# Performance work log

Measured on AMD Instinct MI355X. Metric: run time of the kernel, lower is better.

Reference implementation:

```python
import jax, jax.numpy as jnp
import numpy as np

B, T, S, E, H, V = 64, 72, 72, 128, 256, 32000


def setup_inputs() -> dict:
    key = jax.random.key(0)
    ks = jax.random.split(key, 12)
    scale = 1.0 / np.sqrt(H)
    return {
        "target_tensor": jax.random.randint(ks[0], (B, T), 0, V),
        "encoder_outputs": jax.random.normal(ks[1], (B, S, H), dtype=jnp.float32),
        "encoder_seq_lens": jax.random.randint(ks[2], (B,), 1, S + 1),
        "h0": jax.random.normal(ks[3], (B, H), dtype=jnp.float32),
        "c0": jax.random.normal(ks[4], (B, H), dtype=jnp.float32),
        "emb": jax.random.normal(ks[5], (V, E), dtype=jnp.float32) * 0.05,
        "W_ih": jax.random.uniform(ks[6], (4 * H, E), jnp.float32, -scale, scale),
        "W_hh": jax.random.uniform(ks[7], (4 * H, H), jnp.float32, -scale, scale),
        "b_ih": jax.random.uniform(ks[8], (4 * H,), jnp.float32, -scale, scale),
        "b_hh": jax.random.uniform(ks[9], (4 * H,), jnp.float32, -scale, scale),
        "W_lin": jax.random.uniform(ks[10], (V, 2 * H), jnp.float32, -scale, scale),
        "b_lin": jax.random.uniform(ks[11], (V,), jnp.float32, -scale, scale),
    }


def reference(target_tensor, encoder_outputs, encoder_seq_lens, h0, c0,
              emb, W_ih, W_hh, b_ih, b_hh, W_lin, b_lin):
    # attention mask over encoder positions: (B, S) bool
    mask = jnp.arange(S)[None, :] < encoder_seq_lens[:, None]
    inv_sqrt_h = 1.0 / jnp.sqrt(jnp.asarray(H, jnp.float32))
    bias = b_ih + b_hh

    def step(carry, tok):
        h, c = carry                                   # (B,H) each
        x = emb[tok]                                   # (B,E) embedding lookup
        gates = x @ W_ih.T + h @ W_hh.T + bias         # (B,4H), torch gate order i,f,g,o
        i, f, g, o = jnp.split(gates, 4, axis=-1)
        c_new = jax.nn.sigmoid(f) * c + jax.nn.sigmoid(i) * jnp.tanh(g)
        h_new = jax.nn.sigmoid(o) * jnp.tanh(c_new)    # lstm_output for a 1-step LSTM
        scores = jnp.einsum('bh,bsh->bs', h_new, encoder_outputs) * inv_sqrt_h
        scores = jnp.where(mask, scores, -jnp.inf)
        attn = jax.nn.softmax(scores, axis=-1)         # (B,S)
        ctx = jnp.einsum('bs,bsh->bh', attn, encoder_outputs)
        logits = jnp.concatenate([h_new, ctx], axis=-1) @ W_lin.T + b_lin  # (B,V)
        return (h_new, c_new), logits

    (_, _), outs = jax.lax.scan(step, (h0, c0), target_tensor.T)  # outs: (T,B,V)
    return jnp.transpose(outs, (1, 0, 2))              # (B, T, V)
```

## Files before the change

### kernel.cpp

```cpp
#include <hip/hip_runtime.h>

#define BB 64
#define TT 72
#define SS 72
#define EE 128
#define HH 256
#define VV 32000
#define KK 512
#define NB 4
#define NATTN 64
#define NGEMM 188
#define NCHUNK 36
#define NNT 125
#define NITEM (NCHUNK * NNT)

using f32x4  = __attribute__((ext_vector_type(4))) float;
using short8 = __attribute__((ext_vector_type(8))) short;
typedef unsigned long long u64;

__device__ __forceinline__ unsigned short f2bf(float f) {
  unsigned u = __float_as_uint(f);
  unsigned r = (u + 0x7fffu + ((u >> 16) & 1u)) >> 16;
  return (unsigned short)r;
}
__device__ __forceinline__ float bf2f(unsigned short b) {
  return __uint_as_float(((unsigned)b) << 16);
}
__device__ __forceinline__ float sigm(float x) { return 1.f / (1.f + __expf(-x)); }
__device__ __forceinline__ float tanh_f(float x) { return 1.f - 2.f / (__expf(2.f * x) + 1.f); }

__device__ __forceinline__ float wsum(float v) {
  v += __shfl_xor(v, 1, 64);  v += __shfl_xor(v, 2, 64);  v += __shfl_xor(v, 4, 64);
  v += __shfl_xor(v, 8, 64);  v += __shfl_xor(v, 16, 64); v += __shfl_xor(v, 32, 64);
  return v;
}
__device__ __forceinline__ float wmax(float v) {
  v = fmaxf(v, __shfl_xor(v, 1, 64));  v = fmaxf(v, __shfl_xor(v, 2, 64));
  v = fmaxf(v, __shfl_xor(v, 4, 64));  v = fmaxf(v, __shfl_xor(v, 8, 64));
  v = fmaxf(v, __shfl_xor(v, 16, 64)); v = fmaxf(v, __shfl_xor(v, 32, 64));
  return v;
}
__device__ __forceinline__ void g2l16(const void* g, void* l) {
  __builtin_amdgcn_global_load_lds((const __attribute__((address_space(1))) void*)g,
                                   (__attribute__((address_space(3))) void*)l, 16, 0, 0);
}
__device__ __forceinline__ uint4 pack8(const float4 v0, const float4 v1) {
  uint4 o;
  o.x = f2bf(v0.x) | ((unsigned)f2bf(v0.y) << 16);
  o.y = f2bf(v0.z) | ((unsigned)f2bf(v0.w) << 16);
  o.z = f2bf(v1.x) | ((unsigned)f2bf(v1.y) << 16);
  o.w = f2bf(v1.z) | ((unsigned)f2bf(v1.w) << 16);
  return o;
}
__device__ __forceinline__ u64 aload(const u64* p) {
  return __hip_atomic_load(p, __ATOMIC_RELAXED, __HIP_MEMORY_SCOPE_AGENT);
}
__device__ __forceinline__ void astore(u64* p, u64 v) {
  __hip_atomic_store(p, v, __ATOMIC_RELAXED, __HIP_MEMORY_SCOPE_AGENT);
}

__global__ void prep_kernel(const int* __restrict__ tok, const float* __restrict__ emb,
                            const float* __restrict__ Wlin,
                            uint4* __restrict__ xembt, unsigned short* __restrict__ wlin16) {
  const int bid = blockIdx.x, tid = threadIdx.x;
  if (bid < 18) {
    for (int e = bid * 256 + tid; e < TT * 16 * 64; e += 18 * 256) {
      const int b = e & 63, kcx = (e >> 6) & 15, t = e >> 10;
      const int tk = tok[b * TT + t];
      const float4* s = (const float4*)(emb + (size_t)tk * EE + kcx * 8);
      xembt[e] = pack8(s[0], s[1]);
    }
  } else {
    const int n4 = (VV * KK) / 4;
    for (int i = (bid - 18) * 256 + tid; i < n4; i += 238 * 256) {
      float4 v = ((const float4*)Wlin)[i];
      ushort4 o;
      o.x = f2bf(v.x); o.y = f2bf(v.y); o.z = f2bf(v.z); o.w = f2bf(v.w);
      ((ushort4*)wlin16)[i] = o;
    }
  }
}

__global__ __launch_bounds__(512) void mega_kernel(
    const float* __restrict__ h0, const float* __restrict__ c0,
    const float* __restrict__ Wih, const float* __restrict__ Whh,
    const float* __restrict__ bih, const float* __restrict__ bhh,
    const float* __restrict__ enc, const int* __restrict__ lens,
    const float* __restrict__ blin, const uint4* __restrict__ xembt,
    const unsigned short* __restrict__ wlin16,
    uint4* __restrict__ hex, unsigned int* __restrict__ sync,
    u64* __restrict__ hcat64, float* __restrict__ out) {
  __shared__ __align__(16) char smem[114688];
  __shared__ int s_role;

  const int tid = threadIdx.x;
  unsigned int* flags1 = sync;
  unsigned int* F2     = sync + 8;
  unsigned int* elect  = sync + 96;

  if (tid == 0) {
    unsigned xcd;
    asm volatile("s_getreg_b32 %0, hwreg(20, 0, 8)" : "=s"(xcd));
    xcd &= 7;
    int role = -1;
    const unsigned my = __hip_atomic_fetch_add(elect + xcd, 1u,
                          __ATOMIC_RELAXED, __HIP_MEMORY_SCOPE_AGENT);
    if (my < NB) {
      if (my == NB - 1) {
        unsigned exp = 0;
        __hip_atomic_compare_exchange_strong(elect + 8, &exp, xcd + 1,
            __ATOMIC_RELAXED, __ATOMIC_RELAXED, __HIP_MEMORY_SCOPE_AGENT);
      }
      unsigned wv;
      while ((wv = __hip_atomic_load(elect + 8, __ATOMIC_RELAXED,
                                     __HIP_MEMORY_SCOPE_AGENT)) == 0)
        __builtin_amdgcn_s_sleep(1);
      if (wv == xcd + 1) role = (int)my;
    }
    if (role < 0) {
      const unsigned idx = __hip_atomic_fetch_add(elect + 9, 1u,
                             __ATOMIC_RELAXED, __HIP_MEMORY_SCOPE_AGENT);
      role = (idx < NATTN) ? (100 + (int)idx) : (1000 + (int)(idx - NATTN));
    }
    s_role = role;
  }
  __syncthreads();
  const int role = s_role;

  if (role < NB) {
    const int bk = role;
    uint4* hx = (uint4*)smem;
    uint4* xw = (uint4*)(smem + 49152);
    const int ln = tid & 63, w = tid >> 6;
    const int n16 = ln & 15, kgrp = ln >> 4;
    const int wj = w >> 1, wb = w & 1;
    u64* hexq = (u64*)hex;

    short8 wf[4][8];
    f32x4 biasf[4];
    {
      const int jrow = bk * 64 + wj * 16;
#pragma unroll
      for (int g = 0; g < 4; ++g) {
        const int row = g * HH + jrow + n16;
#pragma unroll
        for (int kt = 0; kt < 8; ++kt) {
          const float* src = Whh + (size_t)row * HH + kt * 32 + kgrp * 8;
          const float4 v0 = ((const float4*)src)[0];
          const float4 v1 = ((const float4*)src)[1];
          short8 wv;
          wv[0]=(short)f2bf(v0.x); wv[1]=(short)f2bf(v0.y); wv[2]=(short)f2bf(v0.z); wv[3]=(short)f2bf(v0.w);
          wv[4]=(short)f2bf(v1.x); wv[5]=(short)f2bf(v1.y); wv[6]=(short)f2bf(v1.z); wv[7]=(short)f2bf(v1.w);
          wf[g][kt] = wv;
        }
        const int r4 = g * HH + jrow + kgrp * 4;
        const float4 bi = *(const float4*)(bih + r4);
        const float4 bh = *(const float4*)(bhh + r4);
        biasf[g] = (f32x4){bi.x + bh.x, bi.y + bh.y, bi.z + bh.z, bi.w + bh.w};
      }
    }
#pragma unroll
    for (int i = 0; i < 8; ++i) {
      const int e = i * 512 + tid;
      const int en = e & 15, ek = (e >> 4) & 3, ewj = (e >> 6) & 3,
                ekt = (e >> 8) & 3, eg = e >> 10;
      const int row = eg * HH + bk * 64 + ewj * 16 + en;
      const float* src = Wih + (size_t)row * EE + ekt * 32 + ek * 8;
      xw[e] = pack8(((const float4*)src)[0], ((const float4*)src)[1]);
    }
    float creg[2][4];
#pragma unroll
    for (int mt = 0; mt < 2; ++mt)
#pragma unroll
      for (int r = 0; r < 4; ++r)
        creg[mt][r] = c0[(size_t)((wb * 2 + mt) * 16 + n16) * HH + bk * 64 + wj * 16 + kgrp * 4 + r];
#pragma unroll
    for (int i = 0; i < 4; ++i) {
      const int e = i * 512 + tid;
      const int kc = e >> 6, b = e & 63;
      const float* src = h0 + (size_t)b * HH + kc * 8;
      hx[kc * 64 + b] = pack8(((const float4*)src)[0], ((const float4*)src)[1]);
    }
    __syncthreads();

    const int kcq  = bk * 8 + wj * 2 + (kgrp >> 1);
    const int half = kgrp & 1;
    const int jq   = bk * 16 + wj * 4 + kgrp;

    for (int t = 0; t < TT; ++t) {
#pragma unroll
      for (int i = 0; i < 2; ++i) {
        const int e = (i * 8 + w) * 64 + ln;
        g2l16(xembt + (size_t)t * 1024 + e, (char*)&hx[32 * 64] + e * 16);
      }
      if (t > 0) {
        if (tid < NB) {
          while (__hip_atomic_load(flags1 + tid, __ATOMIC_RELAXED,
                                   __HIP_MEMORY_SCOPE_AGENT) < (unsigned)t)
            __builtin_amdgcn_s_sleep(1);
        }
        __syncthreads();
#pragma unroll
        for (int i = 0; i < 4; ++i) {
          const int e = (i * 8 + w) * 64 + ln;
          g2l16(hex + (size_t)t * 2048 + e, (char*)hx + e * 16);
        }
      }
      __syncthreads();

      f32x4 acc[4][2];
#pragma unroll
      for (int g = 0; g < 4; ++g)
#pragma unroll
        for (int mt = 0; mt < 2; ++mt)
          acc[g][mt] = biasf[g];

#pragma unroll
      for (int kt = 0; kt < 8; ++kt) {
#pragma unroll
        for (int mt = 0; mt < 2; ++mt) {
          const short8 b = *(const short8*)&hx[(kt * 4 + kgrp) * 64 + (wb * 2 + mt) * 16 + n16];
          acc[0][mt] = __builtin_amdgcn_mfma_f32_16x16x32_bf16(wf[0][kt], b, acc[0][mt], 0, 0, 0);
          acc[1][mt] = __builtin_amdgcn_mfma_f32_16x16x32_bf16(wf[1][kt], b, acc[1][mt], 0, 0, 0);
          acc[2][mt] = __builtin_amdgcn_mfma_f32_16x16x32_bf16(wf[2][kt], b, acc[2][mt], 0, 0, 0);
          acc[3][mt] = __builtin_amdgcn_mfma_f32_16x16x32_bf16(wf[3][kt], b, acc[3][mt], 0, 0, 0);
        }
      }
#pragma unroll
      for (int kti = 0; kti < 4; ++kti) {
        short8 wx[4];
#pragma unroll
        for (int g = 0; g < 4; ++g)
          wx[g] = *(const short8*)&xw[(((g * 4 + kti) * 4 + wj) * 4 + kgrp) * 16 + n16];
#pragma unroll
        for (int mt = 0; mt < 2; ++mt) {
          const short8 b = *(const short8*)&hx[(32 + kti * 4 + kgrp) * 64 + (wb * 2 + mt) * 16 + n16];
#pragma unroll
          for (int g = 0; g < 4; ++g)
            acc[g][mt] = __builtin_amdgcn_mfma_f32_16x16x32_bf16(wx[g], b, acc[g][mt], 0, 0, 0);
        }
      }

#pragma unroll
      for (int mt = 0; mt < 2; ++mt) {
        u64 pk = 0;
#pragma unroll
        for (int r = 0; r < 4; ++r) {
          const float iv = acc[0][mt][r], fv = acc[1][mt][r],
                      gv = acc[2][mt][r], ov = acc[3][mt][r];
          const float cn = sigm(fv) * creg[mt][r] + sigm(iv) * tanh_f(gv);
          creg[mt][r] = cn;
          const float hv = sigm(ov) * tanh_f(cn);
          pk |= (u64)f2bf(hv) << (16 * r);
        }
        const int batch = (wb * 2 + mt) * 16 + n16;
        astore(hexq + ((size_t)((t + 1) * 32 + kcq) * 64 + batch) * 2 + half, pk);
        astore(hcat64 + (size_t)(t * 64 + batch) * 128 + jq, pk);
      }
      asm volatile("s_waitcnt vmcnt(0)" ::: "memory");
      __syncthreads();
      if (tid == 0)
        __hip_atomic_store(flags1 + bk, (unsigned)(t + 1),
                           __ATOMIC_RELAXED, __HIP_MEMORY_SCOPE_AGENT);
    }
  } else if (role < 1000) {
    const int b = role - 100;
    float* enc_s = (float*)smem;
    float* h_s   = (float*)(smem + 73728);
    float* at_s  = (float*)(smem + 74752);
    float* ctx_s = (float*)(smem + 75776);
    const int wv8 = tid >> 6, ln = tid & 63;
    const int len = lens[b];
    const u64* hexq = (const u64*)hex;
    {
      const float4* src = (const float4*)(enc + (size_t)b * SS * HH);
      float4* dst = (float4*)enc_s;
      for (int i = tid; i < SS * HH / 4; i += 512) dst[i] = src[i];
    }
    __syncthreads();

    for (int t = 0; t < TT; ++t) {
      if (tid < NB) {
        while (__hip_atomic_load(flags1 + tid, __ATOMIC_RELAXED,
                                 __HIP_MEMORY_SCOPE_AGENT) < (unsigned)(t + 1))
          __builtin_amdgcn_s_sleep(1);
      }
      __syncthreads();
      if (tid < 64) {
        const int kc = tid >> 1, hf = tid & 1;
        const u64 v = aload(hexq + ((size_t)((t + 1) * 32 + kc) * 64 + b) * 2 + hf);
        const int j0 = kc * 8 + hf * 4;
        h_s[j0]     = bf2f((unsigned short)v);
        h_s[j0 + 1] = bf2f((unsigned short)(v >> 16));
        h_s[j0 + 2] = bf2f((unsigned short)(v >> 32));
        h_s[j0 + 3] = bf2f((unsigned short)(v >> 48));
      }
      __syncthreads();

      const float4 hv = ((const float4*)h_s)[ln];
      for (int s = wv8; s < SS; s += 8) {
        const float4 ev = ((const float4*)(enc_s + s * HH))[ln];
        float p = hv.x * ev.x + hv.y * ev.y + hv.z * ev.z + hv.w * ev.w;
        p = wsum(p);
        if (ln == 0) at_s[s] = p * 0.0625f;
      }
      __syncthreads();
      if (wv8 == 0) {
        const float v0 = (ln < len) ? at_s[ln] : -3.0e38f;
        const bool has1 = (ln < 8) && (64 + ln < len);
        const float v1 = has1 ? at_s[64 + ln] : -3.0e38f;
        const float m = wmax(fmaxf(v0, v1));
        const float e0 = (ln < len) ? __expf(v0 - m) : 0.f;
        const float e1 = has1 ? __expf(v1 - m) : 0.f;
        const float inv = 1.f / wsum(e0 + e1);
        at_s[ln] = e0 * inv;
        if (ln < 8) at_s[64 + ln] = e1 * inv;
      }
      __syncthreads();
      if (tid < HH) {
        float acc = 0.f;
#pragma unroll 8
        for (int s = 0; s < SS; ++s) acc += at_s[s] * enc_s[s * HH + tid];
        ctx_s[tid] = acc;
      }
      __syncthreads();
      if (tid < 64) {
        const u64 pk = (u64)f2bf(ctx_s[tid * 4])
                     | ((u64)f2bf(ctx_s[tid * 4 + 1]) << 16)
                     | ((u64)f2bf(ctx_s[tid * 4 + 2]) << 32)
                     | ((u64)f2bf(ctx_s[tid * 4 + 3]) << 48);
        astore(hcat64 + (size_t)(t * 64 + b) * 128 + 64 + tid, pk);
      }
      asm volatile("s_waitcnt vmcnt(0)" ::: "memory");
      __syncthreads();
      if (tid == 0)
        __hip_atomic_fetch_add(F2 + t, 1u, __ATOMIC_RELAXED, __HIP_MEMORY_SCOPE_AGENT);
    }
  } else {
    const int gid = role - 1000;
    unsigned short* As = (unsigned short*)smem;
    unsigned short* Bs = (unsigned short*)(smem + 8192);
    char* Asb = smem;
    char* Bsb = smem + 8192;
    const int ln = tid & 63, w = tid >> 6;
    const int n16 = ln & 15, kgrp = ln >> 4;
    const int wm = w >> 2, wn = w & 3;
    const int arow = tid >> 3, aq = tid & 7;
    const int o0 = tid * 16;
    const int r0 = o0 >> 6, c0b = o0 & 63;

    for (int it = gid; it < NITEM; it += NGEMM) {
      const int mc = it / NNT, ntile = it % NNT;
      if (tid == 0) {
        while (__hip_atomic_load(F2 + 2 * mc, __ATOMIC_RELAXED, __HIP_MEMORY_SCOPE_AGENT) < NATTN ||
               __hip_atomic_load(F2 + 2 * mc + 1, __ATOMIC_RELAXED, __HIP_MEMORY_SCOPE_AGENT) < NATTN)
          __builtin_amdgcn_s_sleep(2);
      }
      __syncthreads();

      const int m0 = mc * 128, n0 = ntile * 256;
      const char* Bb = (const char*)(wlin16 + (size_t)n0 * KK);
      f32x4 acc[4][4] = {};
      float bs[4];
#pragma unroll
      for (int fn = 0; fn < 4; ++fn) bs[fn] = blin[n0 + wn * 64 + fn * 16 + n16];

      for (int kt = 0; kt < 16; ++kt) {
        const u64 va0 = aload(hcat64 + (size_t)(m0 + arow) * 128 + kt * 8 + aq);
        const u64 va1 = aload(hcat64 + (size_t)(m0 + 64 + arow) * 128 + kt * 8 + aq);
        g2l16(Bb + (size_t)r0 * (KK * 2) + kt * 64 + c0b, Bsb + o0);
        g2l16(Bb + (size_t)(128 + r0) * (KK * 2) + kt * 64 + c0b, Bsb + 8192 + o0);
        asm volatile("s_waitcnt vmcnt(0)" ::: "memory");
        *(u64*)(Asb + arow * 64 + aq * 8) = va0;
        *(u64*)(Asb + 4096 + arow * 64 + aq * 8) = va1;
        __syncthreads();

        short8 af[4], bf[4];
#pragma unroll
        for (int f = 0; f < 4; ++f) {
          af[f] = *(const short8*)&As[(wm * 64 + f * 16 + n16) * 32 + kgrp * 8];
          bf[f] = *(const short8*)&Bs[(wn * 64 + f * 16 + n16) * 32 + kgrp * 8];
        }
#pragma unroll
        for (int fm = 0; fm < 4; ++fm)
#pragma unroll
          for (int fn = 0; fn < 4; ++fn)
            acc[fm][fn] = __builtin_amdgcn_mfma_f32_16x16x32_bf16(af[fm], bf[fn], acc[fm][fn], 0, 0, 0);
        __syncthreads();
      }

#pragma unroll
      for (int fm = 0; fm < 4; ++fm) {
        const int mrow = m0 + wm * 64 + fm * 16 + (ln >> 4) * 4;
        const int trow = mrow >> 6, brow = mrow & 63;
#pragma unroll
        for (int fn = 0; fn < 4; ++fn) {
          const int n = n0 + wn * 64 + fn * 16 + n16;
          float* cp = out + (size_t)(brow * TT + trow) * VV + n;
#pragma unroll
          for (int r = 0; r < 4; ++r) cp[(size_t)r * TT * VV] = acc[fm][fn][r] + bs[fn];
        }
      }
    }
  }
}

extern "C" void kernel_launch(void* const* d_in, const int* in_sizes, int n_in,
                              void* d_out, int out_size, void* d_ws, size_t ws_size,
                              hipStream_t stream) {
  const int*   tok  = (const int*)  d_in[0];
  const float* enc  = (const float*)d_in[1];
  const int*   lens = (const int*)  d_in[2];
  const float* h0   = (const float*)d_in[3];
  const float* c0   = (const float*)d_in[4];
  const float* emb  = (const float*)d_in[5];
  const float* Wih  = (const float*)d_in[6];
  const float* Whh  = (const float*)d_in[7];
  const float* bih  = (const float*)d_in[8];
  const float* bhh  = (const float*)d_in[9];
  const float* Wlin = (const float*)d_in[10];
  const float* blin = (const float*)d_in[11];

  char* ws = (char*)d_ws;
  unsigned short* wlin16 = (unsigned short*)(ws);
  u64*            hcat64 = (u64*)           (ws + 32768000);
  uint4*          xembt  = (uint4*)         (ws + 37486592);
  uint4*          hex    = (uint4*)         (ws + 38666240);
  unsigned int*   sync   = (unsigned int*)  (ws + 41058304);
  float* out = (float*)d_out;

  hipMemsetAsync(sync, 0, 512, stream);
  prep_kernel<<<256, 256, 0, stream>>>(tok, emb, Wlin, xembt, wlin16);
  mega_kernel<<<256, 512, 0, stream>>>(h0, c0, Wih, Whh, bih, bhh, enc, lens,
                                       blin, xembt, wlin16, hex, sync, hcat64, out);
}
```

Baseline: 611.8 us.

## Restructure vocab GEMM per-timestep with resident A tile and double-buffered weights

The output-projection workers now process one timestep (64 batch rows, full K=512) at a time, keeping the whole A tile in swizzled LDS and sweeping five 256-column vocab tiles. Weight tiles are double-buffered with XOR-swizzled layout so the next K slice loads while MFMAs run. Workers wait on a single per-step flag instead of pairs of steps. The h half of the concatenated activation is now written by the attention blocks instead of the LSTM blocks, which shortens the recurrent critical path. The risks are a larger LDS footprint, narrower per-warp N tiles with less weight reuse per block, and the change in which blocks write the h half.

```diff
diff --git a/kernel.cpp b/kernel.cpp
--- a/kernel.cpp
+++ b/kernel.cpp
@@ -10,9 +10,6 @@
 #define NB 4
 #define NATTN 64
 #define NGEMM 188
-#define NCHUNK 36
-#define NNT 125
-#define NITEM (NCHUNK * NNT)
 
 using f32x4  = __attribute__((ext_vector_type(4))) float;
 using short8 = __attribute__((ext_vector_type(8))) short;
@@ -185,7 +182,6 @@
 
     const int kcq  = bk * 8 + wj * 2 + (kgrp >> 1);
     const int half = kgrp & 1;
-    const int jq   = bk * 16 + wj * 4 + kgrp;
 
     for (int t = 0; t < TT; ++t) {
 #pragma unroll
@@ -255,7 +251,6 @@
         }
         const int batch = (wb * 2 + mt) * 16 + n16;
         astore(hexq + ((size_t)((t + 1) * 32 + kcq) * 64 + batch) * 2 + half, pk);
-        astore(hcat64 + (size_t)(t * 64 + batch) * 128 + jq, pk);
       }
       asm volatile("s_waitcnt vmcnt(0)" ::: "memory");
       __syncthreads();
@@ -283,7 +278,7 @@
       if (tid < NB) {
         while (__hip_atomic_load(flags1 + tid, __ATOMIC_RELAXED,
                                  __HIP_MEMORY_SCOPE_AGENT) < (unsigned)(t + 1))
-          __builtin_amdgcn_s_sleep(1);
+          __builtin_amdgcn_s_sleep(2);
       }
       __syncthreads();
       if (tid < 64) {
@@ -294,6 +289,7 @@
         h_s[j0 + 1] = bf2f((unsigned short)(v >> 16));
         h_s[j0 + 2] = bf2f((unsigned short)(v >> 32));
         h_s[j0 + 3] = bf2f((unsigned short)(v >> 48));
+        astore(hcat64 + (size_t)(t * 64 + b) * 128 + tid, v);
       }
       __syncthreads();
 
@@ -338,67 +334,89 @@
     }
   } else {
     const int gid = role - 1000;
-    unsigned short* As = (unsigned short*)smem;
-    unsigned short* Bs = (unsigned short*)(smem + 8192);
-    char* Asb = smem;
-    char* Bsb = smem + 8192;
+    char* Bsb = smem + 65536;
     const int ln = tid & 63, w = tid >> 6;
     const int n16 = ln & 15, kgrp = ln >> 4;
-    const int wm = w >> 2, wn = w & 3;
-    const int arow = tid >> 3, aq = tid & 7;
-    const int o0 = tid * 16;
-    const int r0 = o0 >> 6, c0b = o0 & 63;
-
-    for (int it = gid; it < NITEM; it += NGEMM) {
-      const int mc = it / NNT, ntile = it % NNT;
+    const int lane = gid % 25;
+    const int sub  = gid / 25;
+    const int nbl  = (lane < 13) ? 8 : 7;
+
+    for (int t = sub; t < TT; t += nbl) {
       if (tid == 0) {
-        while (__hip_atomic_load(F2 + 2 * mc, __ATOMIC_RELAXED, __HIP_MEMORY_SCOPE_AGENT) < NATTN ||
-               __hip_atomic_load(F2 + 2 * mc + 1, __ATOMIC_RELAXED, __HIP_MEMORY_SCOPE_AGENT) < NATTN)
-          __builtin_amdgcn_s_sleep(2);
-      }
-      __syncthreads();
-
-      const int m0 = mc * 128, n0 = ntile * 256;
-      const char* Bb = (const char*)(wlin16 + (size_t)n0 * KK);
-      f32x4 acc[4][4] = {};
-      float bs[4];
-#pragma unroll
-      for (int fn = 0; fn < 4; ++fn) bs[fn] = blin[n0 + wn * 64 + fn * 16 + n16];
-
-      for (int kt = 0; kt < 16; ++kt) {
-        const u64 va0 = aload(hcat64 + (size_t)(m0 + arow) * 128 + kt * 8 + aq);
-        const u64 va1 = aload(hcat64 + (size_t)(m0 + 64 + arow) * 128 + kt * 8 + aq);
-        g2l16(Bb + (size_t)r0 * (KK * 2) + kt * 64 + c0b, Bsb + o0);
-        g2l16(Bb + (size_t)(128 + r0) * (KK * 2) + kt * 64 + c0b, Bsb + 8192 + o0);
-        asm volatile("s_waitcnt vmcnt(0)" ::: "memory");
-        *(u64*)(Asb + arow * 64 + aq * 8) = va0;
-        *(u64*)(Asb + 4096 + arow * 64 + aq * 8) = va1;
+        while (__hip_atomic_load(F2 + t, __ATOMIC_RELAXED, __HIP_MEMORY_SCOPE_AGENT) < NATTN)
+          __builtin_amdgcn_s_sleep(8);
+      }
+      __syncthreads();
+
+#pragma unroll
+      for (int i = 0; i < 8; ++i) {
+        const int s = i * 512 + tid;
+        const int row = s >> 6, off = s & 63;
+        const size_t src = (size_t)t * 65536 + ((size_t)row << 10)
+                         + ((size_t)(off ^ (row & 7)) << 4);
+        g2l16((const char*)hcat64 + src, smem + s * 16);
+      }
+
+      for (int nt2 = 0; nt2 < 5; ++nt2) {
+        const int nbase = (lane * 5 + nt2) * 256;
+        float bs[2];
+#pragma unroll
+        for (int fn = 0; fn < 2; ++fn) bs[fn] = blin[nbase + w * 32 + fn * 16 + n16];
+
+#pragma unroll
+        for (int i = 0; i < 2; ++i) {
+          const int s = i * 512 + tid;
+          const int row = s >> 2, sl = s & 3;
+          const size_t src = ((size_t)(nbase + row) << 10) + ((size_t)(sl ^ (row & 3)) << 4);
+          g2l16((const char*)wlin16 + src, Bsb + s * 16);
+        }
         __syncthreads();
 
-        short8 af[4], bf[4];
-#pragma unroll
-        for (int f = 0; f < 4; ++f) {
-          af[f] = *(const short8*)&As[(wm * 64 + f * 16 + n16) * 32 + kgrp * 8];
-          bf[f] = *(const short8*)&Bs[(wn * 64 + f * 16 + n16) * 32 + kgrp * 8];
-        }
-#pragma unroll
-        for (int fm = 0; fm < 4; ++fm)
-#pragma unroll
-          for (int fn = 0; fn < 4; ++fn)
-            acc[fm][fn] = __builtin_amdgcn_mfma_f32_16x16x32_bf16(af[fm], bf[fn], acc[fm][fn], 0, 0, 0);
-        __syncthreads();
-      }
-
-#pragma unroll
-      for (int fm = 0; fm < 4; ++fm) {
-        const int mrow = m0 + wm * 64 + fm * 16 + (ln >> 4) * 4;
-        const int trow = mrow >> 6, brow = mrow & 63;
-#pragma unroll
-        for (int fn = 0; fn < 4; ++fn) {
-          const int n = n0 + wn * 64 + fn * 16 + n16;
-          float* cp = out + (size_t)(brow * TT + trow) * VV + n;
-#pragma unroll
-          for (int r = 0; r < 4; ++r) cp[(size_t)r * TT * VV] = acc[fm][fn][r] + bs[fn];
+        f32x4 acc[4][2] = {};
+        for (int kt = 0; kt < 16; ++kt) {
+          const int cur = kt & 1;
+          if (kt < 15) {
+            const int nxt = cur ^ 1;
+#pragma unroll
+            for (int i = 0; i < 2; ++i) {
+              const int s = i * 512 + tid;
+              const int row = s >> 2, sl = s & 3;
+              const size_t src = ((size_t)(nbase + row) << 10) + (size_t)((kt + 1) << 6)
+                               + ((size_t)(sl ^ (row & 3)) << 4);
+              g2l16((const char*)wlin16 + src, Bsb + nxt * 16384 + s * 16);
+            }
+          }
+          short8 af[4], bf[2];
+#pragma unroll
+          for (int f = 0; f < 4; ++f) {
+            const int row = f * 16 + n16;
+            af[f] = *(const short8*)(smem + (row << 10)
+                      + ((((kt << 2) + kgrp) ^ (row & 7)) << 4));
+          }
+#pragma unroll
+          for (int fn = 0; fn < 2; ++fn) {
+            const int rr = w * 32 + fn * 16 + n16;
+            bf[fn] = *(const short8*)(Bsb + cur * 16384 + (rr << 6)
+                      + ((kgrp ^ (rr & 3)) << 4));
+          }
+#pragma unroll
+          for (int fm = 0; fm < 4; ++fm)
+#pragma unroll
+            for (int fn = 0; fn < 2; ++fn)
+              acc[fm][fn] = __builtin_amdgcn_mfma_f32_16x16x32_bf16(af[fm], bf[fn], acc[fm][fn], 0, 0, 0);
+          __syncthreads();
+        }
+
+#pragma unroll
+        for (int fm = 0; fm < 4; ++fm) {
+          const int b0 = fm * 16 + (ln >> 4) * 4;
+#pragma unroll
+          for (int fn = 0; fn < 2; ++fn) {
+            const int n = nbase + w * 32 + fn * 16 + n16;
+            float* cp = out + ((size_t)b0 * TT + t) * VV + n;
+#pragma unroll
+            for (int r = 0; r < 4; ++r) cp[(size_t)r * TT * VV] = acc[fm][fn][r] + bs[fn];
+          }
         }
       }
     }
```

New measurement: 644.6 us. 5.4% more time.

## Spread LSTM recurrence over 8 blocks and double-buffer wider output GEMM tiles

Applied to the files above, without the earlier changes.

The recurrent LSTM step moves from 4 to 8 blocks on one XCD. Both W_hh and W_ih are held in registers, and the bias is read from LDS, to shorten the serial per-step critical path. The hcat store moves to the attention blocks, and sync flags are padded to separate cache lines. The output-projection GEMM switches to 128x512 tiles with double-buffered, XOR-swizzled LDS loads issued directly from global memory. In exchange it needs more register pressure in the recurrent blocks, more cross-block synchronisation, and bounds checks for the partial last N tile.

```diff
diff --git a/kernel.cpp b/kernel.cpp
--- a/kernel.cpp
+++ b/kernel.cpp
@@ -7,12 +7,11 @@
 #define HH 256
 #define VV 32000
 #define KK 512
-#define NB 4
+#define NB 8
 #define NATTN 64
-#define NGEMM 188
-#define NCHUNK 36
-#define NNT 125
-#define NITEM (NCHUNK * NNT)
+#define NGEMM 184
+#define NNT2 63
+#define NITEM (36 * NNT2)
 
 using f32x4  = __attribute__((ext_vector_type(4))) float;
 using short8 = __attribute__((ext_vector_type(8))) short;
@@ -90,13 +89,13 @@
     const unsigned short* __restrict__ wlin16,
     uint4* __restrict__ hex, unsigned int* __restrict__ sync,
     u64* __restrict__ hcat64, float* __restrict__ out) {
-  __shared__ __align__(16) char smem[114688];
+  __shared__ __align__(16) char smem[90112];
   __shared__ int s_role;
 
   const int tid = threadIdx.x;
   unsigned int* flags1 = sync;
-  unsigned int* F2     = sync + 8;
-  unsigned int* elect  = sync + 96;
+  unsigned int* F2     = sync + 256;
+  unsigned int* elect  = sync + 336;
 
   if (tid == 0) {
     unsigned xcd;
@@ -130,50 +129,40 @@
   if (role < NB) {
     const int bk = role;
     uint4* hx = (uint4*)smem;
-    uint4* xw = (uint4*)(smem + 49152);
+    float* biasL = (float*)(smem + 49152);
     const int ln = tid & 63, w = tid >> 6;
     const int n16 = ln & 15, kgrp = ln >> 4;
-    const int wj = w >> 1, wb = w & 1;
+    const int wj = w >> 2, wb = w & 3;
     u64* hexq = (u64*)hex;
 
-    short8 wf[4][8];
-    f32x4 biasf[4];
+    short8 wf[4][12];
+#pragma unroll
+    for (int g = 0; g < 4; ++g) {
+      const int row = g * HH + bk * 32 + wj * 16 + n16;
+#pragma unroll
+      for (int kt = 0; kt < 12; ++kt) {
+        const float* src = (kt < 8) ? (Whh + (size_t)row * HH + kt * 32 + kgrp * 8)
+                                    : (Wih + (size_t)row * EE + (kt - 8) * 32 + kgrp * 8);
+        const float4 v0 = ((const float4*)src)[0];
+        const float4 v1 = ((const float4*)src)[1];
+        short8 wv;
+        wv[0]=(short)f2bf(v0.x); wv[1]=(short)f2bf(v0.y); wv[2]=(short)f2bf(v0.z); wv[3]=(short)f2bf(v0.w);
+        wv[4]=(short)f2bf(v1.x); wv[5]=(short)f2bf(v1.y); wv[6]=(short)f2bf(v1.z); wv[7]=(short)f2bf(v1.w);
+        wf[g][kt] = wv;
+      }
+    }
+    if (tid < 128) {
+      const int wj2 = tid >> 6, kg2 = (tid >> 4) & 3, g2 = (tid >> 2) & 3, r2 = tid & 3;
+      const int row = g2 * HH + bk * 32 + wj2 * 16 + kg2 * 4 + r2;
+      biasL[tid] = bih[row] + bhh[row];
+    }
+    const int batch = wb * 16 + n16;
+    const int j0 = bk * 32 + wj * 16 + kgrp * 4;
+    float creg[4];
     {
-      const int jrow = bk * 64 + wj * 16;
-#pragma unroll
-      for (int g = 0; g < 4; ++g) {
-        const int row = g * HH + jrow + n16;
-#pragma unroll
-        for (int kt = 0; kt < 8; ++kt) {
-          const float* src = Whh + (size_t)row * HH + kt * 32 + kgrp * 8;
-          const float4 v0 = ((const float4*)src)[0];
-          const float4 v1 = ((const float4*)src)[1];
-          short8 wv;
-          wv[0]=(short)f2bf(v0.x); wv[1]=(short)f2bf(v0.y); wv[2]=(short)f2bf(v0.z); wv[3]=(short)f2bf(v0.w);
-          wv[4]=(short)f2bf(v1.x); wv[5]=(short)f2bf(v1.y); wv[6]=(short)f2bf(v1.z); wv[7]=(short)f2bf(v1.w);
-          wf[g][kt] = wv;
-        }
-        const int r4 = g * HH + jrow + kgrp * 4;
-        const float4 bi = *(const float4*)(bih + r4);
-        const float4 bh = *(const float4*)(bhh + r4);
-        biasf[g] = (f32x4){bi.x + bh.x, bi.y + bh.y, bi.z + bh.z, bi.w + bh.w};
-      }
-    }
-#pragma unroll
-    for (int i = 0; i < 8; ++i) {
-      const int e = i * 512 + tid;
-      const int en = e & 15, ek = (e >> 4) & 3, ewj = (e >> 6) & 3,
-                ekt = (e >> 8) & 3, eg = e >> 10;
-      const int row = eg * HH + bk * 64 + ewj * 16 + en;
-      const float* src = Wih + (size_t)row * EE + ekt * 32 + ek * 8;
-      xw[e] = pack8(((const float4*)src)[0], ((const float4*)src)[1]);
-    }
-    float creg[2][4];
-#pragma unroll
-    for (int mt = 0; mt < 2; ++mt)
-#pragma unroll
-      for (int r = 0; r < 4; ++r)
-        creg[mt][r] = c0[(size_t)((wb * 2 + mt) * 16 + n16) * HH + bk * 64 + wj * 16 + kgrp * 4 + r];
+      const float4 cv = *(const float4*)(c0 + (size_t)batch * HH + j0);
+      creg[0] = cv.x; creg[1] = cv.y; creg[2] = cv.z; creg[3] = cv.w;
+    }
 #pragma unroll
     for (int i = 0; i < 4; ++i) {
       const int e = i * 512 + tid;
@@ -183,84 +172,62 @@
     }
     __syncthreads();
 
-    const int kcq  = bk * 8 + wj * 2 + (kgrp >> 1);
+    const int kcq  = bk * 4 + wj * 2 + (kgrp >> 1);
     const int half = kgrp & 1;
-    const int jq   = bk * 16 + wj * 4 + kgrp;
 
     for (int t = 0; t < TT; ++t) {
 #pragma unroll
       for (int i = 0; i < 2; ++i) {
-        const int e = (i * 8 + w) * 64 + ln;
-        g2l16(xembt + (size_t)t * 1024 + e, (char*)&hx[32 * 64] + e * 16);
+        const int e = i * 512 + w * 64 + ln;
+        g2l16(xembt + (size_t)t * 1024 + e, (char*)hx + (size_t)(2048 + e) * 16);
       }
       if (t > 0) {
         if (tid < NB) {
-          while (__hip_atomic_load(flags1 + tid, __ATOMIC_RELAXED,
+          while (__hip_atomic_load(flags1 + tid * 32, __ATOMIC_RELAXED,
                                    __HIP_MEMORY_SCOPE_AGENT) < (unsigned)t)
             __builtin_amdgcn_s_sleep(1);
         }
         __syncthreads();
 #pragma unroll
         for (int i = 0; i < 4; ++i) {
-          const int e = (i * 8 + w) * 64 + ln;
-          g2l16(hex + (size_t)t * 2048 + e, (char*)hx + e * 16);
-        }
-      }
-      __syncthreads();
-
-      f32x4 acc[4][2];
-#pragma unroll
-      for (int g = 0; g < 4; ++g)
-#pragma unroll
-        for (int mt = 0; mt < 2; ++mt)
-          acc[g][mt] = biasf[g];
-
-#pragma unroll
-      for (int kt = 0; kt < 8; ++kt) {
-#pragma unroll
-        for (int mt = 0; mt < 2; ++mt) {
-          const short8 b = *(const short8*)&hx[(kt * 4 + kgrp) * 64 + (wb * 2 + mt) * 16 + n16];
-          acc[0][mt] = __builtin_amdgcn_mfma_f32_16x16x32_bf16(wf[0][kt], b, acc[0][mt], 0, 0, 0);
-          acc[1][mt] = __builtin_amdgcn_mfma_f32_16x16x32_bf16(wf[1][kt], b, acc[1][mt], 0, 0, 0);
-          acc[2][mt] = __builtin_amdgcn_mfma_f32_16x16x32_bf16(wf[2][kt], b, acc[2][mt], 0, 0, 0);
-          acc[3][mt] = __builtin_amdgcn_mfma_f32_16x16x32_bf16(wf[3][kt], b, acc[3][mt], 0, 0, 0);
-        }
-      }
-#pragma unroll
-      for (int kti = 0; kti < 4; ++kti) {
-        short8 wx[4];
-#pragma unroll
-        for (int g = 0; g < 4; ++g)
-          wx[g] = *(const short8*)&xw[(((g * 4 + kti) * 4 + wj) * 4 + kgrp) * 16 + n16];
-#pragma unroll
-        for (int mt = 0; mt < 2; ++mt) {
-          const short8 b = *(const short8*)&hx[(32 + kti * 4 + kgrp) * 64 + (wb * 2 + mt) * 16 + n16];
-#pragma unroll
-          for (int g = 0; g < 4; ++g)
-            acc[g][mt] = __builtin_amdgcn_mfma_f32_16x16x32_bf16(wx[g], b, acc[g][mt], 0, 0, 0);
-        }
-      }
-
-#pragma unroll
-      for (int mt = 0; mt < 2; ++mt) {
-        u64 pk = 0;
-#pragma unroll
-        for (int r = 0; r < 4; ++r) {
-          const float iv = acc[0][mt][r], fv = acc[1][mt][r],
-                      gv = acc[2][mt][r], ov = acc[3][mt][r];
-          const float cn = sigm(fv) * creg[mt][r] + sigm(iv) * tanh_f(gv);
-          creg[mt][r] = cn;
-          const float hv = sigm(ov) * tanh_f(cn);
-          pk |= (u64)f2bf(hv) << (16 * r);
-        }
-        const int batch = (wb * 2 + mt) * 16 + n16;
-        astore(hexq + ((size_t)((t + 1) * 32 + kcq) * 64 + batch) * 2 + half, pk);
-        astore(hcat64 + (size_t)(t * 64 + batch) * 128 + jq, pk);
-      }
+          const int e = i * 512 + w * 64 + ln;
+          g2l16(hex + (size_t)t * 2048 + e, (char*)hx + (size_t)e * 16);
+        }
+      }
+      __syncthreads();
+
+      f32x4 a0 = {0,0,0,0}, a1 = a0, a2 = a0, a3 = a0;
+#pragma unroll
+      for (int kt = 0; kt < 12; ++kt) {
+        const short8 b = *(const short8*)&hx[(kt * 4 + kgrp) * 64 + batch];
+        a0 = __builtin_amdgcn_mfma_f32_16x16x32_bf16(wf[0][kt], b, a0, 0, 0, 0);
+        a1 = __builtin_amdgcn_mfma_f32_16x16x32_bf16(wf[1][kt], b, a1, 0, 0, 0);
+        a2 = __builtin_amdgcn_mfma_f32_16x16x32_bf16(wf[2][kt], b, a2, 0, 0, 0);
+        a3 = __builtin_amdgcn_mfma_f32_16x16x32_bf16(wf[3][kt], b, a3, 0, 0, 0);
+      }
+      const float4 b0 = *(const float4*)&biasL[wj * 64 + kgrp * 16 + 0];
+      const float4 b1 = *(const float4*)&biasL[wj * 64 + kgrp * 16 + 4];
+      const float4 b2 = *(const float4*)&biasL[wj * 64 + kgrp * 16 + 8];
+      const float4 b3 = *(const float4*)&biasL[wj * 64 + kgrp * 16 + 12];
+      const float bi[4] = {b0.x, b0.y, b0.z, b0.w};
+      const float bf_[4] = {b1.x, b1.y, b1.z, b1.w};
+      const float bg[4] = {b2.x, b2.y, b2.z, b2.w};
+      const float bo[4] = {b3.x, b3.y, b3.z, b3.w};
+      u64 pk = 0;
+#pragma unroll
+      for (int r = 0; r < 4; ++r) {
+        const float iv = a0[r] + bi[r], fv = a1[r] + bf_[r],
+                    gv = a2[r] + bg[r], ov = a3[r] + bo[r];
+        const float cn = sigm(fv) * creg[r] + sigm(iv) * tanh_f(gv);
+        creg[r] = cn;
+        const float hv = sigm(ov) * tanh_f(cn);
+        pk |= (u64)f2bf(hv) << (16 * r);
+      }
+      astore(hexq + ((size_t)(t + 1) * 2048 + kcq * 64 + batch) * 2 + half, pk);
       asm volatile("s_waitcnt vmcnt(0)" ::: "memory");
       __syncthreads();
       if (tid == 0)
-        __hip_atomic_store(flags1 + bk, (unsigned)(t + 1),
+        __hip_atomic_store(flags1 + bk * 32, (unsigned)(t + 1),
                            __ATOMIC_RELAXED, __HIP_MEMORY_SCOPE_AGENT);
     }
   } else if (role < 1000) {
@@ -281,19 +248,20 @@
 
     for (int t = 0; t < TT; ++t) {
       if (tid < NB) {
-        while (__hip_atomic_load(flags1 + tid, __ATOMIC_RELAXED,
+        while (__hip_atomic_load(flags1 + tid * 32, __ATOMIC_RELAXED,
                                  __HIP_MEMORY_SCOPE_AGENT) < (unsigned)(t + 1))
           __builtin_amdgcn_s_sleep(1);
       }
       __syncthreads();
       if (tid < 64) {
         const int kc = tid >> 1, hf = tid & 1;
-        const u64 v = aload(hexq + ((size_t)((t + 1) * 32 + kc) * 64 + b) * 2 + hf);
+        const u64 v = aload(hexq + ((size_t)(t + 1) * 2048 + kc * 64 + b) * 2 + hf);
         const int j0 = kc * 8 + hf * 4;
         h_s[j0]     = bf2f((unsigned short)v);
         h_s[j0 + 1] = bf2f((unsigned short)(v >> 16));
         h_s[j0 + 2] = bf2f((unsigned short)(v >> 32));
         h_s[j0 + 3] = bf2f((unsigned short)(v >> 48));
+        astore(hcat64 + (size_t)(t * 64 + b) * 128 + tid, v);
       }
       __syncthreads();
 
@@ -338,67 +306,89 @@
     }
   } else {
     const int gid = role - 1000;
-    unsigned short* As = (unsigned short*)smem;
-    unsigned short* Bs = (unsigned short*)(smem + 8192);
-    char* Asb = smem;
-    char* Bsb = smem + 8192;
+    char* AsB = smem;
+    char* BsB = smem + 16384;
     const int ln = tid & 63, w = tid >> 6;
     const int n16 = ln & 15, kgrp = ln >> 4;
     const int wm = w >> 2, wn = w & 3;
-    const int arow = tid >> 3, aq = tid & 7;
-    const int o0 = tid * 16;
-    const int r0 = o0 >> 6, c0b = o0 & 63;
 
     for (int it = gid; it < NITEM; it += NGEMM) {
-      const int mc = it / NNT, ntile = it % NNT;
-      if (tid == 0) {
-        while (__hip_atomic_load(F2 + 2 * mc, __ATOMIC_RELAXED, __HIP_MEMORY_SCOPE_AGENT) < NATTN ||
-               __hip_atomic_load(F2 + 2 * mc + 1, __ATOMIC_RELAXED, __HIP_MEMORY_SCOPE_AGENT) < NATTN)
-          __builtin_amdgcn_s_sleep(2);
-      }
-      __syncthreads();
-
-      const int m0 = mc * 128, n0 = ntile * 256;
-      const char* Bb = (const char*)(wlin16 + (size_t)n0 * KK);
-      f32x4 acc[4][4] = {};
-      float bs[4];
-#pragma unroll
-      for (int fn = 0; fn < 4; ++fn) bs[fn] = blin[n0 + wn * 64 + fn * 16 + n16];
-
+      const int mc = it / NNT2, ntl = it % NNT2;
+      if (tid < 2) {
+        while (__hip_atomic_load(F2 + 2 * mc + tid, __ATOMIC_RELAXED,
+                                 __HIP_MEMORY_SCOPE_AGENT) < NATTN)
+          __builtin_amdgcn_s_sleep(8);
+      }
+      __syncthreads();
+      const int m0 = mc * 128, n0 = ntl * 512;
+      float bs[8];
+#pragma unroll
+      for (int f = 0; f < 8; ++f) {
+        const int n = n0 + wn * 128 + f * 16 + n16;
+        bs[f] = (n < VV) ? blin[n] : 0.f;
+      }
+      {
+        const int row = tid >> 2, sl = tid & 3;
+        g2l16((const char*)hcat64 + (size_t)(m0 + row) * 1024 + ((sl ^ (row & 3)) << 4),
+              AsB + tid * 16);
+      }
+#pragma unroll
+      for (int i = 0; i < 4; ++i) {
+        const int e = i * 512 + tid, row = e >> 2, sl = e & 3;
+        g2l16((const char*)wlin16 + (size_t)(n0 + row) * 1024 + ((sl ^ (row & 3)) << 4),
+              BsB + e * 16);
+      }
+      __syncthreads();
+
+      f32x4 acc[4][8] = {};
       for (int kt = 0; kt < 16; ++kt) {
-        const u64 va0 = aload(hcat64 + (size_t)(m0 + arow) * 128 + kt * 8 + aq);
-        const u64 va1 = aload(hcat64 + (size_t)(m0 + 64 + arow) * 128 + kt * 8 + aq);
-        g2l16(Bb + (size_t)r0 * (KK * 2) + kt * 64 + c0b, Bsb + o0);
-        g2l16(Bb + (size_t)(128 + r0) * (KK * 2) + kt * 64 + c0b, Bsb + 8192 + o0);
-        asm volatile("s_waitcnt vmcnt(0)" ::: "memory");
-        *(u64*)(Asb + arow * 64 + aq * 8) = va0;
-        *(u64*)(Asb + 4096 + arow * 64 + aq * 8) = va1;
-        __syncthreads();
-
-        short8 af[4], bf[4];
+        const int cur = kt & 1;
+        if (kt < 15) {
+          const int nb = cur ^ 1;
+          const int kb = (kt + 1) * 64;
+          {
+            const int row = tid >> 2, sl = tid & 3;
+            g2l16((const char*)hcat64 + (size_t)(m0 + row) * 1024 + kb + ((sl ^ (row & 3)) << 4),
+                  AsB + nb * 8192 + tid * 16);
+          }
+#pragma unroll
+          for (int i = 0; i < 4; ++i) {
+            const int e = i * 512 + tid, row = e >> 2, sl = e & 3;
+            g2l16((const char*)wlin16 + (size_t)(n0 + row) * 1024 + kb + ((sl ^ (row & 3)) << 4),
+                  BsB + nb * 32768 + e * 16);
+          }
+        }
+        short8 af[4], bf[8];
 #pragma unroll
         for (int f = 0; f < 4; ++f) {
-          af[f] = *(const short8*)&As[(wm * 64 + f * 16 + n16) * 32 + kgrp * 8];
-          bf[f] = *(const short8*)&Bs[(wn * 64 + f * 16 + n16) * 32 + kgrp * 8];
+          const int row = wm * 64 + f * 16 + n16;
+          af[f] = *(const short8*)(AsB + cur * 8192 + row * 64 + ((kgrp ^ (row & 3)) << 4));
+        }
+#pragma unroll
+        for (int f = 0; f < 8; ++f) {
+          const int row = wn * 128 + f * 16 + n16;
+          bf[f] = *(const short8*)(BsB + cur * 32768 + row * 64 + ((kgrp ^ (row & 3)) << 4));
         }
 #pragma unroll
         for (int fm = 0; fm < 4; ++fm)
 #pragma unroll
-          for (int fn = 0; fn < 4; ++fn)
+          for (int fn = 0; fn < 8; ++fn)
             acc[fm][fn] = __builtin_amdgcn_mfma_f32_16x16x32_bf16(af[fm], bf[fn], acc[fm][fn], 0, 0, 0);
         __syncthreads();
       }
 
+      const int trow = mc * 2 + wm;
 #pragma unroll
       for (int fm = 0; fm < 4; ++fm) {
-        const int mrow = m0 + wm * 64 + fm * 16 + (ln >> 4) * 4;
-        const int trow = mrow >> 6, brow = mrow & 63;
-#pragma unroll
-        for (int fn = 0; fn < 4; ++fn) {
-          const int n = n0 + wn * 64 + fn * 16 + n16;
-          float* cp = out + (size_t)(brow * TT + trow) * VV + n;
-#pragma unroll
-          for (int r = 0; r < 4; ++r) cp[(size_t)r * TT * VV] = acc[fm][fn][r] + bs[fn];
+        const int b0 = fm * 16 + kgrp * 4;
+#pragma unroll
+        for (int fn = 0; fn < 8; ++fn) {
+          const int n = n0 + wn * 128 + fn * 16 + n16;
+          if (n < VV) {
+            float* cp = out + ((size_t)b0 * TT + trow) * VV + n;
+#pragma unroll
+            for (int r = 0; r < 4; ++r) cp[(size_t)r * TT * VV] = acc[fm][fn][r] + bs[fn];
+          }
         }
       }
     }
@@ -423,13 +413,13 @@
 
   char* ws = (char*)d_ws;
   unsigned short* wlin16 = (unsigned short*)(ws);
-  u64*            hcat64 = (u64*)           (ws + 32768000);
-  uint4*          xembt  = (uint4*)         (ws + 37486592);
-  uint4*          hex    = (uint4*)         (ws + 38666240);
-  unsigned int*   sync   = (unsigned int*)  (ws + 41058304);
+  u64*            hcat64 = (u64*)           (ws + 33030144);
+  uint4*          xembt  = (uint4*)         (ws + 37748736);
+  uint4*          hex    = (uint4*)         (ws + 38928384);
+  unsigned int*   sync   = (unsigned int*)  (ws + 41320448);
   float* out = (float*)d_out;
 
-  hipMemsetAsync(sync, 0, 512, stream);
+  hipMemsetAsync(sync, 0, 2048, stream);
   prep_kernel<<<256, 256, 0, stream>>>(tok, emb, Wlin, xembt, wlin16);
   mega_kernel<<<256, 512, 0, stream>>>(h0, c0, Wih, Whh, bih, bhh, enc, lens,
                                        blin, xembt, wlin16, hex, sync, hcat64, out);
```

New measurement: 546.4 us. 1.12x faster.
